# Performance work log

Measured on AMD Instinct MI355X. Metric: run time of the kernel, lower is better.

Reference implementation:

```python
import jax, jax.numpy as jnp
import numpy as np

S = 64.0   # scale (default s)
M = 0.5    # angular margin (default m)
EPS = 1e-07
N, D, C = 2048, 128, 100000

def setup_inputs() -> dict:
    key = jax.random.key(0)
    kx, kw, kl = jax.random.split(key, 3)
    x = jax.random.normal(kx, (N, D), dtype=jnp.float32)
    # NOTE: the torch module never actually normalizes W (local rebinding bug),
    # so W is a raw linear weight. Small init keeps exp(s*wf) finite.
    W = jax.random.normal(kw, (C, D), dtype=jnp.float32) * 0.01
    labels = jax.random.randint(kl, (N,), 0, C, dtype=jnp.int64)
    return {"x": x, "W": W, "labels": labels}

def reference(x, W, labels):
    # L2-normalize embeddings only (matches original: weight normalize is a no-op)
    x_n = x / jnp.linalg.norm(x, axis=1, keepdims=True)
    wf = jnp.einsum('nd,cd->nc', x_n, W)                      # [N, C] logits
    tgt = jnp.take_along_axis(wf, labels[:, None], axis=1)[:, 0]  # wf[i, y_i]
    tgt = jnp.clip(tgt, -1.0 + EPS, 1.0 - EPS)
    numerator = S * jnp.cos(jnp.arccos(tgt) + M)              # margin logit
    # sum over j != y_i of exp(s * wf_ij)
    exp_all = jnp.exp(S * wf)
    excl_sum = jnp.sum(exp_all, axis=1) - jnp.take_along_axis(exp_all, labels[:, None], axis=1)[:, 0]
    denominator = jnp.exp(numerator) + excl_sum
    L = numerator - jnp.log(denominator)
    return -jnp.mean(L)
```

## Files before the change

### kernel.cpp

```cpp
#include <hip/hip_runtime.h>
#include <math.h>

typedef __attribute__((ext_vector_type(8))) short s16x8;
typedef __attribute__((ext_vector_type(4))) float f32x4;

#define N_ROWS 2048
#define D_DIM  128
#define N_CLS  100000
#define N_TILES 782
#define N_PAD   96.0f
#define S_SCALE 64.0f
#define S_LOG2E 92.33248261689366f
#define EPS_F   1e-7f
#define COS_M   0.8775825618903728f
#define SIN_M   0.479425538604203f

#if __has_builtin(__builtin_amdgcn_exp2f)
#define EXP2F(x) __builtin_amdgcn_exp2f(x)
#else
#define EXP2F(x) exp2f(x)
#endif

__device__ __forceinline__ unsigned int f2bf1(float f) {
    unsigned int u = __float_as_uint(f);
    return (u + 0x7FFFu + ((u >> 16) & 1u)) >> 16;
}
__device__ __forceinline__ unsigned int f2bf2(float lo, float hi) {
    return f2bf1(lo) | (f2bf1(hi) << 16);
}

__global__ __launch_bounds__(256)
void k_normalize(const float* __restrict__ x, const float* __restrict__ W,
                 const int* __restrict__ labels,
                 float* __restrict__ tgt, uint4* __restrict__ xb2) {
    const int gt = blockIdx.x;
    const int t = threadIdx.x;
    const int rr = t >> 1, h = t & 1;
    const int row = gt * 128 + rr;

    const f32x4* src = (const f32x4*)(x + (size_t)row * D_DIM + h * 64);
    f32x4 v[16];
    float s = 0.f;
    #pragma unroll
    for (int q = 0; q < 16; q++) {
        v[q] = src[q];
        s += v[q][0]*v[q][0] + v[q][1]*v[q][1] + v[q][2]*v[q][2] + v[q][3]*v[q][3];
    }
    s += __shfl_xor(s, 1);
    const float inv = 1.0f / sqrtf(s);

    const int y = labels[row];
    const f32x4* wsrc = (const f32x4*)(W + (size_t)y * D_DIM + h * 64);
    float d = 0.f;
    #pragma unroll
    for (int q = 0; q < 16; q++) {
        f32x4 w = wsrc[q];
        d += v[q][0]*w[0] + v[q][1]*w[1] + v[q][2]*w[2] + v[q][3]*w[3];
    }
    d += __shfl_xor(d, 1);
    if (h == 0) tgt[row] = d * inv;

    const float invs = inv * S_LOG2E;
    #pragma unroll
    for (int q = 0; q < 16; q++) {
        v[q][0] *= invs; v[q][1] *= invs; v[q][2] *= invs; v[q][3] *= invs;
    }

    const int wn = rr >> 6, j = (rr >> 4) & 3, lr = rr & 15;
    #pragma unroll
    for (int q2 = 0; q2 < 8; q2++) {
        const int ck = h * 8 + q2;
        const int ks = ck >> 2, lk = ck & 3;
        const int idx = gt * 2048 + wn * 1024 + j * 256 + ks * 64 + lk * 16 + lr;
        f32x4 f0 = v[q2 * 2], f1 = v[q2 * 2 + 1];
        xb2[idx] = make_uint4(f2bf2(f0[0], f0[1]), f2bf2(f0[2], f0[3]),
                              f2bf2(f1[0], f1[1]), f2bf2(f1[2], f1[3]));
    }
}

#define MFMA16(ACC, BUF) do {                                                 \
    ACC##0 = (f32x4){0.f,0.f,0.f,0.f}; ACC##1 = (f32x4){0.f,0.f,0.f,0.f};     \
    ACC##2 = (f32x4){0.f,0.f,0.f,0.f}; ACC##3 = (f32x4){0.f,0.f,0.f,0.f};     \
    _Pragma("unroll")                                                         \
    for (int ks_ = 0; ks_ < 4; ks_++) {                                       \
        const s16x8 b_ = *(const s16x8*)&BUF[ks_];                            \
        ACC##0 = __builtin_amdgcn_mfma_f32_16x16x32_bf16(a_[ks_][0], b_, ACC##0, 0, 0, 0); \
        ACC##1 = __builtin_amdgcn_mfma_f32_16x16x32_bf16(a_[ks_][1], b_, ACC##1, 0, 0, 0); \
        ACC##2 = __builtin_amdgcn_mfma_f32_16x16x32_bf16(a_[ks_][2], b_, ACC##2, 0, 0, 0); \
        ACC##3 = __builtin_amdgcn_mfma_f32_16x16x32_bf16(a_[ks_][3], b_, ACC##3, 0, 0, 0); \
    }                                                                         \
} while (0)

#define RELOAD(BUF, J) do {                                                   \
    if (it < 15) {                                                            \
        _Pragma("unroll")                                                     \
        for (int ks_ = 0; ks_ < 4; ks_++)                                     \
            BUF[ks_] = bbase[(it + 1) * 2048 + (J) * 256 + ks_ * 64];         \
    }                                                                         \
} while (0)

#define EXPST(ACC, ITE, JE) do {                                              \
    f32x4 pv;                                                                 \
    _Pragma("unroll")                                                         \
    for (int r_ = 0; r_ < 4; r_++)                                            \
        pv[r_] = (EXP2F(ACC##0[r_]) + EXP2F(ACC##1[r_]))                      \
               + (EXP2F(ACC##2[r_]) + EXP2F(ACC##3[r_]));                     \
    float pj = (pv[0] + pv[1]) + (pv[2] + pv[3]);                             \
    pj += __shfl_xor(pj, 16);                                                 \
    pj += __shfl_xor(pj, 32);                                                 \
    if ((lane >> 4) == 0)                                                     \
        psum[wm][ITE][wn * 64 + (JE) * 16 + lr] = pj;                         \
} while (0)

__global__ __launch_bounds__(256, 3)
void k_main(const uint4* __restrict__ xb2, const float* __restrict__ W,
            float* __restrict__ rowsum) {
    __shared__ uint4 Wsh[2048];
    __shared__ float psum[2][16][128];
    const int t = threadIdx.x;
    const int c0 = blockIdx.x * 128;

    #pragma unroll
    for (int m = 0; m < 8; m++) {
        const int idx = m * 256 + t;
        const int flr = idx & 15, lk = (idx >> 4) & 3;
        const int ks = (idx >> 6) & 3, fi = (idx >> 8) & 3, fwm = idx >> 10;
        const int cls = c0 + fwm * 64 + fi * 16 + flr;
        const int k0 = (ks * 4 + lk) * 8;
        uint4 val = make_uint4(0u, 0u, 0u, 0u);
        if (cls < N_CLS) {
            const f32x4* g = (const f32x4*)(W + (size_t)cls * D_DIM + k0);
            f32x4 f0 = g[0], f1 = g[1];
            val.x = f2bf2(f0[0], f0[1]); val.y = f2bf2(f0[2], f0[3]);
            val.z = f2bf2(f1[0], f1[1]); val.w = f2bf2(f1[2], f1[3]);
        }
        Wsh[idx] = val;
    }
    __syncthreads();

    const int lane = t & 63;
    const int wid = t >> 6;
    const int wm = wid >> 1;
    const int wn = wid & 1;
    const int lr = lane & 15;
    const uint4* bbase = xb2 + wn * 1024 + lane;

    uint4 b0[4], b1[4], b2[4], b3[4];
    s16x8 a_[4][4];
    f32x4 accA0, accA1, accA2, accA3;
    f32x4 accB0, accB1, accB2, accB3;

    #pragma unroll
    for (int ks = 0; ks < 4; ks++) {
        b0[ks] = bbase[0 * 256 + ks * 64];
        b1[ks] = bbase[1 * 256 + ks * 64];
        b2[ks] = bbase[2 * 256 + ks * 64];
        b3[ks] = bbase[3 * 256 + ks * 64];
    }

    for (int it = 0; it < 16; it++) {
        #pragma unroll
        for (int ks = 0; ks < 4; ks++)
            #pragma unroll
            for (int i = 0; i < 4; i++)
                a_[ks][i] = *(const s16x8*)&Wsh[wm * 1024 + i * 256 + ks * 64 + lane];
        if (it) EXPST(accB, it - 1, 3);
        MFMA16(accA, b0);  RELOAD(b0, 0);
        MFMA16(accB, b1);  RELOAD(b1, 1);  EXPST(accA, it, 0);
        MFMA16(accA, b2);  RELOAD(b2, 2);  EXPST(accB, it, 1);
        MFMA16(accB, b3);  RELOAD(b3, 3);  EXPST(accA, it, 2);
    }
    EXPST(accB, 15, 3);

    __syncthreads();
    #pragma unroll
    for (int k = 0; k < 8; k++) {
        const int flat = t + k * 256;
        const int it = flat >> 7, r = flat & 127;
        atomicAdd(&rowsum[it * 128 + r], psum[0][it][r] + psum[1][it][r]);
    }
}

__global__ void k_final(const float* __restrict__ rowsum, const float* __restrict__ tgt,
                        float* __restrict__ out) {
    int t = threadIdx.x;
    float lsum = 0.f;
    for (int i = t; i < N_ROWS; i += 256) {
        float tr = tgt[i];
        float tc = fminf(fmaxf(tr, -1.f + EPS_F), 1.f - EPS_F);
        float num = S_SCALE * (tc * COS_M - sqrtf(fmaxf(1.f - tc * tc, 0.f)) * SIN_M);
        float excl = rowsum[i] - N_PAD - __expf(S_SCALE * tr);
        float den = __expf(num) + excl;
        lsum += num - logf(den);
    }
    #pragma unroll
    for (int off = 1; off < 64; off <<= 1) lsum += __shfl_xor(lsum, off);
    __shared__ float wsums[4];
    if ((t & 63) == 0) wsums[t >> 6] = lsum;
    __syncthreads();
    if (t == 0) out[0] = -(wsums[0] + wsums[1] + wsums[2] + wsums[3]) / (float)N_ROWS;
}

extern "C" void kernel_launch(void* const* d_in, const int* in_sizes, int n_in,
                              void* d_out, int out_size, void* d_ws, size_t ws_size,
                              hipStream_t stream) {
    const float* x = (const float*)d_in[0];
    const float* W = (const float*)d_in[1];
    const int* labels = (const int*)d_in[2];
    float* out = (float*)d_out;

    uint4* xb2    = (uint4*)d_ws;
    float* rowsum = (float*)((char*)xb2 + (size_t)N_ROWS * D_DIM * 2);
    float* tgt    = rowsum + N_ROWS;

    hipMemsetAsync(rowsum, 0, N_ROWS * sizeof(float), stream);
    k_normalize<<<N_ROWS / 128, 256, 0, stream>>>(x, W, labels, tgt, xb2);
    k_main<<<N_TILES, 256, 0, stream>>>(xb2, W, rowsum);
    k_final<<<1, 256, 0, stream>>>(rowsum, tgt, out);
}
```

Before: 96.23 us.

## Balance main-kernel work with fractional tile/row-chunk units over a fixed grid

The main kernel no longer launches one block per 128-class tile. It splits the work into 3128 units (782 tiles × 4 row quarters) and hands each of 768 blocks an even contiguous range of about 4.07 units, so the tail wave of 782 tiles over 768 slots is evened out. Blocks may then reload a W tile for partial row ranges, which adds some extra W conversion work and more synchronisation. Separately, the normalize kernel uses 8 threads per row and 64 blocks instead of 16, which gives it more parallelism.

```diff
diff --git a/kernel.cpp b/kernel.cpp
--- a/kernel.cpp
+++ b/kernel.cpp
@@ -8,6 +8,8 @@
 #define D_DIM  128
 #define N_CLS  100000
 #define N_TILES 782
+#define N_UNITS 3128
+#define GRID_MAIN 768
 #define N_PAD   96.0f
 #define S_SCALE 64.0f
 #define S_LOG2E 92.33248261689366f
@@ -33,46 +35,46 @@
 void k_normalize(const float* __restrict__ x, const float* __restrict__ W,
                  const int* __restrict__ labels,
                  float* __restrict__ tgt, uint4* __restrict__ xb2) {
-    const int gt = blockIdx.x;
     const int t = threadIdx.x;
-    const int rr = t >> 1, h = t & 1;
-    const int row = gt * 128 + rr;
-
-    const f32x4* src = (const f32x4*)(x + (size_t)row * D_DIM + h * 64);
-    f32x4 v[16];
+    const int row = blockIdx.x * 32 + (t >> 3);
+    const int p = t & 7;
+
+    const f32x4* src = (const f32x4*)(x + (size_t)row * D_DIM + p * 16);
+    f32x4 v[4];
     float s = 0.f;
     #pragma unroll
-    for (int q = 0; q < 16; q++) {
+    for (int q = 0; q < 4; q++) {
         v[q] = src[q];
         s += v[q][0]*v[q][0] + v[q][1]*v[q][1] + v[q][2]*v[q][2] + v[q][3]*v[q][3];
     }
-    s += __shfl_xor(s, 1);
+    s += __shfl_xor(s, 1); s += __shfl_xor(s, 2); s += __shfl_xor(s, 4);
     const float inv = 1.0f / sqrtf(s);
 
     const int y = labels[row];
-    const f32x4* wsrc = (const f32x4*)(W + (size_t)y * D_DIM + h * 64);
+    const f32x4* wsrc = (const f32x4*)(W + (size_t)y * D_DIM + p * 16);
     float d = 0.f;
     #pragma unroll
-    for (int q = 0; q < 16; q++) {
+    for (int q = 0; q < 4; q++) {
         f32x4 w = wsrc[q];
         d += v[q][0]*w[0] + v[q][1]*w[1] + v[q][2]*w[2] + v[q][3]*w[3];
     }
-    d += __shfl_xor(d, 1);
-    if (h == 0) tgt[row] = d * inv;
+    d += __shfl_xor(d, 1); d += __shfl_xor(d, 2); d += __shfl_xor(d, 4);
+    if (p == 0) tgt[row] = d * inv;
 
     const float invs = inv * S_LOG2E;
     #pragma unroll
-    for (int q = 0; q < 16; q++) {
+    for (int q = 0; q < 4; q++) {
         v[q][0] *= invs; v[q][1] *= invs; v[q][2] *= invs; v[q][3] *= invs;
     }
 
-    const int wn = rr >> 6, j = (rr >> 4) & 3, lr = rr & 15;
-    #pragma unroll
-    for (int q2 = 0; q2 < 8; q2++) {
-        const int ck = h * 8 + q2;
+    const int gt = row >> 7, rr = row & 127;
+    const int wn = rr >> 6, j = (rr >> 4) & 3, lrr = rr & 15;
+    #pragma unroll
+    for (int c2 = 0; c2 < 2; c2++) {
+        const int ck = p * 2 + c2;
         const int ks = ck >> 2, lk = ck & 3;
-        const int idx = gt * 2048 + wn * 1024 + j * 256 + ks * 64 + lk * 16 + lr;
-        f32x4 f0 = v[q2 * 2], f1 = v[q2 * 2 + 1];
+        const int idx = gt * 2048 + wn * 1024 + j * 256 + ks * 64 + lk * 16 + lrr;
+        f32x4 f0 = v[c2 * 2], f1 = v[c2 * 2 + 1];
         xb2[idx] = make_uint4(f2bf2(f0[0], f0[1]), f2bf2(f0[2], f0[3]),
                               f2bf2(f1[0], f1[1]), f2bf2(f1[2], f1[3]));
     }
@@ -92,7 +94,7 @@
 } while (0)
 
 #define RELOAD(BUF, J) do {                                                   \
-    if (it < 15) {                                                            \
+    if (it + 1 < itN) {                                                       \
         _Pragma("unroll")                                                     \
         for (int ks_ = 0; ks_ < 4; ks_++)                                     \
             BUF[ks_] = bbase[(it + 1) * 2048 + (J) * 256 + ks_ * 64];         \
@@ -118,25 +120,9 @@
     __shared__ uint4 Wsh[2048];
     __shared__ float psum[2][16][128];
     const int t = threadIdx.x;
-    const int c0 = blockIdx.x * 128;
-
-    #pragma unroll
-    for (int m = 0; m < 8; m++) {
-        const int idx = m * 256 + t;
-        const int flr = idx & 15, lk = (idx >> 4) & 3;
-        const int ks = (idx >> 6) & 3, fi = (idx >> 8) & 3, fwm = idx >> 10;
-        const int cls = c0 + fwm * 64 + fi * 16 + flr;
-        const int k0 = (ks * 4 + lk) * 8;
-        uint4 val = make_uint4(0u, 0u, 0u, 0u);
-        if (cls < N_CLS) {
-            const f32x4* g = (const f32x4*)(W + (size_t)cls * D_DIM + k0);
-            f32x4 f0 = g[0], f1 = g[1];
-            val.x = f2bf2(f0[0], f0[1]); val.y = f2bf2(f0[2], f0[3]);
-            val.z = f2bf2(f1[0], f1[1]); val.w = f2bf2(f1[2], f1[3]);
-        }
-        Wsh[idx] = val;
-    }
-    __syncthreads();
+    const int b = blockIdx.x;
+    const int u1 = ((b + 1) * 391) / 96;
+    int u = (b * 391) / 96;
 
     const int lane = t & 63;
     const int wid = t >> 6;
@@ -145,39 +131,66 @@
     const int lr = lane & 15;
     const uint4* bbase = xb2 + wn * 1024 + lane;
 
-    uint4 b0[4], b1[4], b2[4], b3[4];
-    s16x8 a_[4][4];
-    f32x4 accA0, accA1, accA2, accA3;
-    f32x4 accB0, accB1, accB2, accB3;
-
-    #pragma unroll
-    for (int ks = 0; ks < 4; ks++) {
-        b0[ks] = bbase[0 * 256 + ks * 64];
-        b1[ks] = bbase[1 * 256 + ks * 64];
-        b2[ks] = bbase[2 * 256 + ks * 64];
-        b3[ks] = bbase[3 * 256 + ks * 64];
-    }
-
-    for (int it = 0; it < 16; it++) {
+    while (u < u1) {
+        const int tile = u >> 2;
+        const int uend = min(u1, (tile + 1) * 4);
+        const int it0 = (u - tile * 4) * 4;
+        const int itN = (uend - tile * 4) * 4;
+        const int c0 = tile * 128;
+
         #pragma unroll
-        for (int ks = 0; ks < 4; ks++)
+        for (int m = 0; m < 8; m++) {
+            const int idx = m * 256 + t;
+            const int flr = idx & 15, lk = (idx >> 4) & 3;
+            const int ks = (idx >> 6) & 3, fi = (idx >> 8) & 3, fwm = idx >> 10;
+            const int cls = c0 + fwm * 64 + fi * 16 + flr;
+            const int k0 = (ks * 4 + lk) * 8;
+            uint4 val = make_uint4(0u, 0u, 0u, 0u);
+            if (cls < N_CLS) {
+                const f32x4* g = (const f32x4*)(W + (size_t)cls * D_DIM + k0);
+                f32x4 f0 = g[0], f1 = g[1];
+                val.x = f2bf2(f0[0], f0[1]); val.y = f2bf2(f0[2], f0[3]);
+                val.z = f2bf2(f1[0], f1[1]); val.w = f2bf2(f1[2], f1[3]);
+            }
+            Wsh[idx] = val;
+        }
+        __syncthreads();
+
+        uint4 b0[4], b1[4], b2[4], b3[4];
+        s16x8 a_[4][4];
+        f32x4 accA0, accA1, accA2, accA3;
+        f32x4 accB0, accB1, accB2, accB3;
+
+        #pragma unroll
+        for (int ks = 0; ks < 4; ks++) {
+            b0[ks] = bbase[it0 * 2048 + 0 * 256 + ks * 64];
+            b1[ks] = bbase[it0 * 2048 + 1 * 256 + ks * 64];
+            b2[ks] = bbase[it0 * 2048 + 2 * 256 + ks * 64];
+            b3[ks] = bbase[it0 * 2048 + 3 * 256 + ks * 64];
+        }
+
+        for (int it = it0; it < itN; it++) {
             #pragma unroll
-            for (int i = 0; i < 4; i++)
-                a_[ks][i] = *(const s16x8*)&Wsh[wm * 1024 + i * 256 + ks * 64 + lane];
-        if (it) EXPST(accB, it - 1, 3);
-        MFMA16(accA, b0);  RELOAD(b0, 0);
-        MFMA16(accB, b1);  RELOAD(b1, 1);  EXPST(accA, it, 0);
-        MFMA16(accA, b2);  RELOAD(b2, 2);  EXPST(accB, it, 1);
-        MFMA16(accB, b3);  RELOAD(b3, 3);  EXPST(accA, it, 2);
-    }
-    EXPST(accB, 15, 3);
-
-    __syncthreads();
-    #pragma unroll
-    for (int k = 0; k < 8; k++) {
-        const int flat = t + k * 256;
-        const int it = flat >> 7, r = flat & 127;
-        atomicAdd(&rowsum[it * 128 + r], psum[0][it][r] + psum[1][it][r]);
+            for (int ks = 0; ks < 4; ks++)
+                #pragma unroll
+                for (int i = 0; i < 4; i++)
+                    a_[ks][i] = *(const s16x8*)&Wsh[wm * 1024 + i * 256 + ks * 64 + lane];
+            if (it > it0) EXPST(accB, it - 1, 3);
+            MFMA16(accA, b0);  RELOAD(b0, 0);
+            MFMA16(accB, b1);  RELOAD(b1, 1);  EXPST(accA, it, 0);
+            MFMA16(accA, b2);  RELOAD(b2, 2);  EXPST(accB, it, 1);
+            MFMA16(accB, b3);  RELOAD(b3, 3);  EXPST(accA, it, 2);
+        }
+        EXPST(accB, itN - 1, 3);
+
+        __syncthreads();
+        const int cnt = (itN - it0) * 128;
+        for (int f = t; f < cnt; f += 256) {
+            const int itg = it0 + (f >> 7), r = f & 127;
+            atomicAdd(&rowsum[itg * 128 + r], psum[0][itg][r] + psum[1][itg][r]);
+        }
+        __syncthreads();
+        u = uend;
     }
 }
 
@@ -214,7 +227,7 @@
     float* tgt    = rowsum + N_ROWS;
 
     hipMemsetAsync(rowsum, 0, N_ROWS * sizeof(float), stream);
-    k_normalize<<<N_ROWS / 128, 256, 0, stream>>>(x, W, labels, tgt, xb2);
-    k_main<<<N_TILES, 256, 0, stream>>>(xb2, W, rowsum);
+    k_normalize<<<N_ROWS / 32, 256, 0, stream>>>(x, W, labels, tgt, xb2);
+    k_main<<<GRID_MAIN, 256, 0, stream>>>(xb2, W, rowsum);
     k_final<<<1, 256, 0, stream>>>(rowsum, tgt, out);
 }
```

Result: slower. 117.6 us (+22.2%).
